# Performance work log

Hardware: AMD Instinct MI355X
Metric: run time of the kernel (lower is better)

## Reference

```python
import jax, jax.numpy as jnp
import numpy as np

B, C, H, W = 16, 192, 96, 96
FILTERS = (1, 3, 3, 3, 3, 1)  # (1,) + filters + (1,)
INIT_SCALE = 8.0
LIKELIHOOD_BOUND = 1e-9


def setup_inputs() -> dict:
    key = jax.random.key(0)
    ks = jax.random.split(key, 3)
    inp = {}
    inp["inputs"] = jax.random.normal(ks[0], (B, C, H, W), dtype=jnp.float32) * 4.0
    # uniform(-0.5, 0.5) quantization noise, supplied explicitly for determinism
    inp["noise"] = jax.random.uniform(ks[1], (B, C, H, W), dtype=jnp.float32) - 0.5
    scale = INIT_SCALE ** (1.0 / (len(FILTERS) - 1))  # 8 ** (1/5)
    for i in range(5):
        fin, fout = FILTERS[i], FILTERS[i + 1]
        init_m = float(np.log(np.expm1(1.0 / scale / fout)))
        inp[f"m{i}"] = jnp.full((C, fout, fin), init_m, dtype=jnp.float32)
        inp[f"b{i}"] = jax.random.uniform(
            jax.random.fold_in(ks[2], i), (C, fout, 1), dtype=jnp.float32,
            minval=-0.5, maxval=0.5)
        inp[f"f{i}"] = jnp.zeros((C, fout, 1), dtype=jnp.float32)
    return inp


@jax.custom_vjp
def low_bound(x):
    return jnp.clip(x, LIKELIHOOD_BOUND, None)

def _lb_fwd(x):
    return jnp.clip(x, LIKELIHOOD_BOUND, None), x

def _lb_bwd(x, g):
    # torch Low_bound: grad zeroed where x < 1e-9 (the t-mask is redundant after zeroing)
    return (jnp.where(x >= LIKELIHOOD_BOUND, g, jnp.zeros_like(g)),)

low_bound.defvjp(_lb_fwd, _lb_bwd)


def _logits_cumulative(x, mats, biases, factors):
    # x: (C, 1, N); each layer: batched tiny matmul + bias + tanh-factor gate
    for m, b, f in zip(mats, biases, factors):
        x = jnp.matmul(jax.nn.softplus(m), x) + b  # (C, f_out, N)
        x = x + jnp.tanh(f) * jnp.tanh(x)
    return x


def reference(inputs, noise, m0, m1, m2, m3, m4,
              b0, b1, b2, b3, b4, f0, f1, f2, f3, f4):
    mats = (m0, m1, m2, m3, m4)
    biases = (b0, b1, b2, b3, b4)
    factors = (f0, f1, f2, f3, f4)
    # permute (B,C,H,W) -> (C,B,H,W) -> (C, 1, B*H*W)
    x = jnp.transpose(inputs, (1, 0, 2, 3)).reshape(C, 1, -1)
    n = jnp.transpose(noise, (1, 0, 2, 3)).reshape(C, 1, -1)
    v = x + n  # 'noise' quantize mode
    lower = _logits_cumulative(v - 0.5, mats, biases, factors)
    upper = _logits_cumulative(v + 0.5, mats, biases, factors)
    sign = jax.lax.stop_gradient(-jnp.sign(lower + upper))
    likelihood = jnp.abs(jax.nn.sigmoid(sign * upper) - jax.nn.sigmoid(sign * lower))
    likelihood = low_bound(likelihood)
    outputs = jnp.transpose(v.reshape(C, B, H, W), (1, 0, 2, 3))
    likelihood = jnp.transpose(likelihood.reshape(C, B, H, W), (1, 0, 2, 3))
    return outputs, likelihood
```

## Files before the change

### kernel.cpp

```cpp
#include <hip/hip_runtime.h>
#include <math.h>

#define CC 192
#define BB 16
#define HWp 9216
#define NPLANES (BB * CC)
#define NELEM (BB * CC * HWp)

#define KLUT 2048
#define VMIN (-30.0f)
#define VMAX (30.0f)
#define DXLUT ((VMAX - VMIN) / (float)(KLUT - 1))
#define INV_DX ((float)(KLUT - 1) / (VMAX - VMIN))
#define OFFLUT (-VMIN * INV_DX)

__device__ __forceinline__ float fast_tanh(float x) {
    float e = __builtin_amdgcn_exp2f(x * 2.8853900817779268f);
    return 1.0f - 2.0f * __builtin_amdgcn_rcpf(e + 1.0f);
}

__device__ __forceinline__ float fast_sigmoid(float z) {
    float e = __builtin_amdgcn_exp2f(z * -1.4426950408889634f);
    return __builtin_amdgcn_rcpf(1.0f + e);
}

__device__ __forceinline__ float softplus_f(float x) {
    return (x > 20.0f) ? x : log1pf(expf(x));
}

struct Params {
    float W0[3], B0[3], T0[3];
    float W1[9], B1[3], T1[3];
    float W2[9], B2[3], T2[3];
    float W3[9], B3[3], T3[3];
    float W4[3], B4, T4;
};

#define EB_LAYER(OUT, IN, W, Bv, Tv)                                          \
    _Pragma("unroll")                                                         \
    for (int j = 0; j < 3; ++j) {                                             \
        float acc = fmaf((W)[j * 3 + 2], (IN)[2],                             \
                    fmaf((W)[j * 3 + 1], (IN)[1],                             \
                    fmaf((W)[j * 3 + 0], (IN)[0], (Bv)[j])));                 \
        (OUT)[j] = acc + (Tv)[j] * fast_tanh(acc);                            \
    }

__device__ __forceinline__ float chain(float u, const Params& P) {
    float h0[3], h1[3], h2[3], h3[3];
#pragma unroll
    for (int j = 0; j < 3; ++j) {
        float a = fmaf(P.W0[j], u, P.B0[j]);
        h0[j] = a + P.T0[j] * fast_tanh(a);
    }
    EB_LAYER(h1, h0, P.W1, P.B1, P.T1);
    EB_LAYER(h2, h1, P.W2, P.B2, P.T2);
    EB_LAYER(h3, h2, P.W3, P.B3, P.T3);
    float y = fmaf(P.W4[2], h3[2], fmaf(P.W4[1], h3[1], fmaf(P.W4[0], h3[0], P.B4)));
    y += P.T4 * fast_tanh(y);
    return y;
}

__device__ __forceinline__ float table_value(float v, const Params& P) {
    float lo = chain(v - 0.5f, P);
    float up = chain(v + 0.5f, P);
    float lk = fabsf(fast_sigmoid(up) - fast_sigmoid(lo));
    return fmaxf(lk, 1e-9f);
}

__device__ __forceinline__ void stage_params(
    int c, int t, float* sP,
    const float* m0, const float* b0, const float* f0,
    const float* m1, const float* b1, const float* f1,
    const float* m2, const float* b2, const float* f2,
    const float* m3, const float* b3, const float* f3,
    const float* m4, const float* b4, const float* f4)
{
    if (t < 59) {
        float val;
        if (t < 9) {
            int j = t % 3, w = t / 3;
            val = (w == 0) ? softplus_f(m0[c * 3 + j])
                : (w == 1) ? b0[c * 3 + j]
                           : tanhf(f0[c * 3 + j]);
        } else if (t < 54) {
            int u = t - 9;
            int l = u / 15, r = u % 15;
            const float* mm = (l == 0) ? m1 : (l == 1) ? m2 : m3;
            const float* bb = (l == 0) ? b1 : (l == 1) ? b2 : b3;
            const float* ff = (l == 0) ? f1 : (l == 1) ? f2 : f3;
            val = (r < 9)  ? softplus_f(mm[c * 9 + r])
                : (r < 12) ? bb[c * 3 + (r - 9)]
                           : tanhf(ff[c * 3 + (r - 12)]);
        } else {
            int r = t - 54;
            val = (r < 3)  ? softplus_f(m4[c * 3 + r])
                : (r == 3) ? b4[c]
                           : tanhf(f4[c]);
        }
        sP[t] = val;
    }
}

__device__ __forceinline__ void load_params(const float* sP, Params& P) {
#pragma unroll
    for (int j = 0; j < 3; ++j) { P.W0[j] = sP[j]; P.B0[j] = sP[3 + j]; P.T0[j] = sP[6 + j]; }
#pragma unroll
    for (int j = 0; j < 9; ++j) { P.W1[j] = sP[9 + j]; P.W2[j] = sP[24 + j]; P.W3[j] = sP[39 + j]; }
#pragma unroll
    for (int j = 0; j < 3; ++j) {
        P.B1[j] = sP[18 + j]; P.T1[j] = sP[21 + j];
        P.B2[j] = sP[33 + j]; P.T2[j] = sP[36 + j];
        P.B3[j] = sP[48 + j]; P.T3[j] = sP[51 + j];
        P.W4[j] = sP[54 + j];
    }
    P.B4 = sP[57];
    P.T4 = sP[58];
}

__device__ __forceinline__ float lut_lookup(const float* sT, float v) {
    float u = fmaf(v, INV_DX, OFFLUT);
    u = fminf(fmaxf(u, 0.0f), (float)(KLUT - 2) + 0.999f);
    float fi = floorf(u);
    float fr = u - fi;
    int i = (int)fi;
    float y0 = sT[i];
    float y1 = sT[i + 1];
    return fmaf(fr, y1 - y0, y0);
}

__global__ __launch_bounds__(256) void build_table(
    const float* __restrict__ m0, const float* __restrict__ b0, const float* __restrict__ f0,
    const float* __restrict__ m1, const float* __restrict__ b1, const float* __restrict__ f1,
    const float* __restrict__ m2, const float* __restrict__ b2, const float* __restrict__ f2,
    const float* __restrict__ m3, const float* __restrict__ b3, const float* __restrict__ f3,
    const float* __restrict__ m4, const float* __restrict__ b4, const float* __restrict__ f4,
    float* __restrict__ tab)
{
    const int c = blockIdx.x;
    const int t = threadIdx.x;
    __shared__ float sP[59];
    stage_params(c, t, sP, m0, b0, f0, m1, b1, f1, m2, b2, f2, m3, b3, f3, m4, b4, f4);
    __syncthreads();
    Params P;
    load_params(sP, P);
    for (int i = t; i < KLUT; i += 256) {
        float v = VMIN + (float)i * DXLUT;
        tab[(size_t)c * KLUT + i] = table_value(v, P);
    }
}

__global__ __launch_bounds__(256) void eb_main(
    const float* __restrict__ x, const float* __restrict__ nz,
    const float* __restrict__ tab, float* __restrict__ out)
{
    const int plane = blockIdx.x;
    const int c = plane % CC;
    const int t = threadIdx.x;

    __shared__ float sT[KLUT];
    {
        const float4* tv = (const float4*)(tab + (size_t)c * KLUT);
        float4* sv = (float4*)sT;
#pragma unroll
        for (int i = 0; i < KLUT / 4 / 256; ++i)
            sv[t + i * 256] = tv[t + i * 256];
    }
    __syncthreads();

    const size_t base = (size_t)plane * HWp;
    const float4* xv = (const float4*)(x + base);
    const float4* nv = (const float4*)(nz + base);
    float4* ov = (float4*)(out + base);
    float4* lv = (float4*)(out + (size_t)NELEM + base);

    for (int i = t; i < HWp / 4; i += 256) {
        float4 a = xv[i];
        float4 n = nv[i];
        float4 v, lk;
        v.x = a.x + n.x;  v.y = a.y + n.y;  v.z = a.z + n.z;  v.w = a.w + n.w;
        lk.x = lut_lookup(sT, v.x);
        lk.y = lut_lookup(sT, v.y);
        lk.z = lut_lookup(sT, v.z);
        lk.w = lut_lookup(sT, v.w);
        ov[i] = v;
        lv[i] = lk;
    }
}

__global__ __launch_bounds__(256) void eb_fused(
    const float* __restrict__ x, const float* __restrict__ nz,
    const float* __restrict__ m0, const float* __restrict__ b0, const float* __restrict__ f0,
    const float* __restrict__ m1, const float* __restrict__ b1, const float* __restrict__ f1,
    const float* __restrict__ m2, const float* __restrict__ b2, const float* __restrict__ f2,
    const float* __restrict__ m3, const float* __restrict__ b3, const float* __restrict__ f3,
    const float* __restrict__ m4, const float* __restrict__ b4, const float* __restrict__ f4,
    float* __restrict__ out)
{
    const int plane = blockIdx.x;
    const int c = plane % CC;
    const int t = threadIdx.x;

    __shared__ float sP[59];
    __shared__ float sT[KLUT];
    stage_params(c, t, sP, m0, b0, f0, m1, b1, f1, m2, b2, f2, m3, b3, f3, m4, b4, f4);
    __syncthreads();
    {
        Params P;
        load_params(sP, P);
#pragma unroll
        for (int k = 0; k < KLUT / 256; ++k) {
            int i = t + k * 256;
            float v = VMIN + (float)i * DXLUT;
            sT[i] = table_value(v, P);
        }
    }
    __syncthreads();

    const size_t base = (size_t)plane * HWp;
    const float4* xv = (const float4*)(x + base);
    const float4* nv = (const float4*)(nz + base);
    float4* ov = (float4*)(out + base);
    float4* lv = (float4*)(out + (size_t)NELEM + base);

    for (int i = t; i < HWp / 4; i += 256) {
        float4 a = xv[i];
        float4 n = nv[i];
        float4 v, lk;
        v.x = a.x + n.x;  v.y = a.y + n.y;  v.z = a.z + n.z;  v.w = a.w + n.w;
        lk.x = lut_lookup(sT, v.x);
        lk.y = lut_lookup(sT, v.y);
        lk.z = lut_lookup(sT, v.z);
        lk.w = lut_lookup(sT, v.w);
        ov[i] = v;
        lv[i] = lk;
    }
}

extern "C" void kernel_launch(void* const* d_in, const int* in_sizes, int n_in,
                              void* d_out, int out_size, void* d_ws, size_t ws_size,
                              hipStream_t stream) {
    const float* x  = (const float*)d_in[0];
    const float* nz = (const float*)d_in[1];
    const float* m0 = (const float*)d_in[2];
    const float* b0 = (const float*)d_in[3];
    const float* f0 = (const float*)d_in[4];
    const float* m1 = (const float*)d_in[5];
    const float* b1 = (const float*)d_in[6];
    const float* f1 = (const float*)d_in[7];
    const float* m2 = (const float*)d_in[8];
    const float* b2 = (const float*)d_in[9];
    const float* f2 = (const float*)d_in[10];
    const float* m3 = (const float*)d_in[11];
    const float* b3 = (const float*)d_in[12];
    const float* f3 = (const float*)d_in[13];
    const float* m4 = (const float*)d_in[14];
    const float* b4 = (const float*)d_in[15];
    const float* f4 = (const float*)d_in[16];
    float* out = (float*)d_out;

    const size_t tab_bytes = (size_t)CC * KLUT * sizeof(float);
    if (ws_size >= tab_bytes) {
        float* tab = (float*)d_ws;
        build_table<<<CC, 256, 0, stream>>>(
            m0, b0, f0, m1, b1, f1, m2, b2, f2, m3, b3, f3, m4, b4, f4, tab);
        eb_main<<<NPLANES, 256, 0, stream>>>(x, nz, tab, out);
    } else {
        eb_fused<<<NPLANES, 256, 0, stream>>>(x, nz,
            m0, b0, f0, m1, b1, f1, m2, b2, f2, m3, b3, f3, m4, b4, f4, out);
    }
}
```

Baseline: 419.1 us.

## Pair LUT entries, halve table size, process two planes per block with nontemporal IO

Shrinks the lookup table to 1024 entries and stores each entry as an adjacent (y0,y1) float2 pair, so every interpolation needs one LDS read instead of two. The main kernel now uses a 2D grid in which each block handles two batch planes of the same channel, so the table is staged into LDS half as many times. Loads and stores become nontemporal vector accesses with a fixed-trip, partially unrolled loop. The coarser table lowers interpolation accuracy, and there are fewer, larger blocks in the grid.

New measurement: 400.7 us. -4.4%, faster.

```diff
diff --git a/kernel.cpp b/kernel.cpp
--- a/kernel.cpp
+++ b/kernel.cpp
@@ -7,12 +7,14 @@
 #define NPLANES (BB * CC)
 #define NELEM (BB * CC * HWp)
 
-#define KLUT 2048
+#define KLUT 1024
 #define VMIN (-30.0f)
 #define VMAX (30.0f)
 #define DXLUT ((VMAX - VMIN) / (float)(KLUT - 1))
 #define INV_DX ((float)(KLUT - 1) / (VMAX - VMIN))
 #define OFFLUT (-VMIN * INV_DX)
+
+typedef float fvec4 __attribute__((ext_vector_type(4)));
 
 __device__ __forceinline__ float fast_tanh(float x) {
     float e = __builtin_amdgcn_exp2f(x * 2.8853900817779268f);
@@ -117,15 +119,13 @@
     P.T4 = sP[58];
 }
 
-__device__ __forceinline__ float lut_lookup(const float* sT, float v) {
+__device__ __forceinline__ float lut_lookup(const float2* sT, float v) {
     float u = fmaf(v, INV_DX, OFFLUT);
-    u = fminf(fmaxf(u, 0.0f), (float)(KLUT - 2) + 0.999f);
+    u = fminf(fmaxf(u, 0.0f), (float)(KLUT - 1));
     float fi = floorf(u);
     float fr = u - fi;
-    int i = (int)fi;
-    float y0 = sT[i];
-    float y1 = sT[i + 1];
-    return fmaf(fr, y1 - y0, y0);
+    float2 y = sT[(int)fi];
+    return fmaf(fr, y.y - y.x, y.x);
 }
 
 __global__ __launch_bounds__(256) void build_table(
@@ -134,56 +134,79 @@
     const float* __restrict__ m2, const float* __restrict__ b2, const float* __restrict__ f2,
     const float* __restrict__ m3, const float* __restrict__ b3, const float* __restrict__ f3,
     const float* __restrict__ m4, const float* __restrict__ b4, const float* __restrict__ f4,
-    float* __restrict__ tab)
+    float2* __restrict__ tab2)
 {
     const int c = blockIdx.x;
     const int t = threadIdx.x;
     __shared__ float sP[59];
+    __shared__ float sY[KLUT];
     stage_params(c, t, sP, m0, b0, f0, m1, b1, f1, m2, b2, f2, m3, b3, f3, m4, b4, f4);
     __syncthreads();
     Params P;
     load_params(sP, P);
-    for (int i = t; i < KLUT; i += 256) {
-        float v = VMIN + (float)i * DXLUT;
-        tab[(size_t)c * KLUT + i] = table_value(v, P);
+#pragma unroll
+    for (int k = 0; k < KLUT / 256; ++k) {
+        int i = t + k * 256;
+        sY[i] = table_value(VMIN + (float)i * DXLUT, P);
+    }
+    __syncthreads();
+#pragma unroll
+    for (int k = 0; k < KLUT / 256; ++k) {
+        int i = t + k * 256;
+        float y0 = sY[i];
+        float y1 = sY[(i + 1 < KLUT) ? i + 1 : KLUT - 1];
+        tab2[(size_t)c * KLUT + i] = make_float2(y0, y1);
     }
 }
 
 __global__ __launch_bounds__(256) void eb_main(
     const float* __restrict__ x, const float* __restrict__ nz,
-    const float* __restrict__ tab, float* __restrict__ out)
-{
-    const int plane = blockIdx.x;
-    const int c = plane % CC;
+    const float2* __restrict__ tab2, float* __restrict__ out)
+{
+    const int c = blockIdx.x;
+    const int q = blockIdx.y;
     const int t = threadIdx.x;
 
-    __shared__ float sT[KLUT];
+    __shared__ float2 sT[KLUT];
     {
-        const float4* tv = (const float4*)(tab + (size_t)c * KLUT);
-        float4* sv = (float4*)sT;
-#pragma unroll
-        for (int i = 0; i < KLUT / 4 / 256; ++i)
-            sv[t + i * 256] = tv[t + i * 256];
-    }
-    __syncthreads();
-
-    const size_t base = (size_t)plane * HWp;
-    const float4* xv = (const float4*)(x + base);
-    const float4* nv = (const float4*)(nz + base);
-    float4* ov = (float4*)(out + base);
-    float4* lv = (float4*)(out + (size_t)NELEM + base);
-
-    for (int i = t; i < HWp / 4; i += 256) {
-        float4 a = xv[i];
-        float4 n = nv[i];
-        float4 v, lk;
-        v.x = a.x + n.x;  v.y = a.y + n.y;  v.z = a.z + n.z;  v.w = a.w + n.w;
-        lk.x = lut_lookup(sT, v.x);
-        lk.y = lut_lookup(sT, v.y);
-        lk.z = lut_lookup(sT, v.z);
-        lk.w = lut_lookup(sT, v.w);
-        ov[i] = v;
-        lv[i] = lk;
+        const fvec4* tv = (const fvec4*)(tab2 + (size_t)c * KLUT);
+        fvec4* sv = (fvec4*)sT;
+#pragma unroll
+        for (int k = 0; k < (KLUT * 2 / 4) / 256; ++k)
+            sv[t + k * 256] = tv[t + k * 256];
+    }
+    __syncthreads();
+
+    const size_t base0 = ((size_t)(2 * q) * CC + c) * HWp;
+    const size_t base1 = base0 + (size_t)CC * HWp;
+
+    const fvec4* xv0 = (const fvec4*)(x + base0);
+    const fvec4* nv0 = (const fvec4*)(nz + base0);
+    fvec4* ov0 = (fvec4*)(out + base0);
+    fvec4* lv0 = (fvec4*)(out + (size_t)NELEM + base0);
+    const fvec4* xv1 = (const fvec4*)(x + base1);
+    const fvec4* nv1 = (const fvec4*)(nz + base1);
+    fvec4* ov1 = (fvec4*)(out + base1);
+    fvec4* lv1 = (fvec4*)(out + (size_t)NELEM + base1);
+
+#pragma unroll 3
+    for (int k = 0; k < (HWp / 4) / 256; ++k) {
+        int i = t + k * 256;
+        fvec4 a0 = __builtin_nontemporal_load(xv0 + i);
+        fvec4 n0 = __builtin_nontemporal_load(nv0 + i);
+        fvec4 a1 = __builtin_nontemporal_load(xv1 + i);
+        fvec4 n1 = __builtin_nontemporal_load(nv1 + i);
+        fvec4 v0 = a0 + n0;
+        fvec4 v1 = a1 + n1;
+        fvec4 l0, l1;
+        l0.x = lut_lookup(sT, v0.x);  l0.y = lut_lookup(sT, v0.y);
+        l0.z = lut_lookup(sT, v0.z);  l0.w = lut_lookup(sT, v0.w);
+        l1.x = lut_lookup(sT, v1.x);  l1.y = lut_lookup(sT, v1.y);
+        l1.z = lut_lookup(sT, v1.z);  l1.w = lut_lookup(sT, v1.w);
+        __builtin_nontemporal_store(v0, ov0 + i);
+        __builtin_nontemporal_store(l0, lv0 + i);
+        __builtin_nontemporal_store(v1, ov1 + i);
+        __builtin_nontemporal_store(l1, lv1 + i);
     }
 }
 
@@ -201,7 +224,8 @@
     const int t = threadIdx.x;
 
     __shared__ float sP[59];
-    __shared__ float sT[KLUT];
+    __shared__ float sY[KLUT];
+    __shared__ float2 sT[KLUT];
     stage_params(c, t, sP, m0, b0, f0, m1, b1, f1, m2, b2, f2, m3, b3, f3, m4, b4, f4);
     __syncthreads();
     {
@@ -210,29 +234,33 @@
 #pragma unroll
         for (int k = 0; k < KLUT / 256; ++k) {
             int i = t + k * 256;
-            float v = VMIN + (float)i * DXLUT;
-            sT[i] = table_value(v, P);
+            sY[i] = table_value(VMIN + (float)i * DXLUT, P);
         }
     }
     __syncthreads();
+#pragma unroll
+    for (int k = 0; k < KLUT / 256; ++k) {
+        int i = t + k * 256;
+        sT[i] = make_float2(sY[i], sY[(i + 1 < KLUT) ? i + 1 : KLUT - 1]);
+    }
+    __syncthreads();
 
     const size_t base = (size_t)plane * HWp;
-    const float4* xv = (const float4*)(x + base);
-    const float4* nv = (const float4*)(nz + base);
-    float4* ov = (float4*)(out + base);
-    float4* lv = (float4*)(out + (size_t)NELEM + base);
-
-    for (int i = t; i < HWp / 4; i += 256) {
-        float4 a = xv[i];
-        float4 n = nv[i];
-        float4 v, lk;
-        v.x = a.x + n.x;  v.y = a.y + n.y;  v.z = a.z + n.z;  v.w = a.w + n.w;
-        lk.x = lut_lookup(sT, v.x);
-        lk.y = lut_lookup(sT, v.y);
-        lk.z = lut_lookup(sT, v.z);
-        lk.w = lut_lookup(sT, v.w);
-        ov[i] = v;
-        lv[i] = lk;
+    const fvec4* xv = (const fvec4*)(x + base);
+    const fvec4* nv = (const fvec4*)(nz + base);
+    fvec4* ov = (fvec4*)(out + base);
+    fvec4* lv = (fvec4*)(out + (size_t)NELEM + base);
+
+    for (int k = 0; k < (HWp / 4) / 256; ++k) {
+        int i = t + k * 256;
+        fvec4 a = __builtin_nontemporal_load(xv + i);
+        fvec4 n = __builtin_nontemporal_load(nv + i);
+        fvec4 v = a + n;
+        fvec4 lk;
+        lk.x = lut_lookup(sT, v.x);  lk.y = lut_lookup(sT, v.y);
+        lk.z = lut_lookup(sT, v.z);  lk.w = lut_lookup(sT, v.w);
+        __builtin_nontemporal_store(v, ov + i);
+        __builtin_nontemporal_store(lk, lv + i);
     }
 }
 
@@ -258,12 +286,12 @@
     const float* f4 = (const float*)d_in[16];
     float* out = (float*)d_out;
 
-    const size_t tab_bytes = (size_t)CC * KLUT * sizeof(float);
+    const size_t tab_bytes = (size_t)CC * KLUT * sizeof(float2);
     if (ws_size >= tab_bytes) {
-        float* tab = (float*)d_ws;
+        float2* tab2 = (float2*)d_ws;
         build_table<<<CC, 256, 0, stream>>>(
-            m0, b0, f0, m1, b1, f1, m2, b2, f2, m3, b3, f3, m4, b4, f4, tab);
-        eb_main<<<NPLANES, 256, 0, stream>>>(x, nz, tab, out);
+            m0, b0, f0, m1, b1, f1, m2, b2, f2, m3, b3, f3, m4, b4, f4, tab2);
+        eb_main<<<dim3(CC, BB / 2), 256, 0, stream>>>(x, nz, tab2, out);
     } else {
         eb_fused<<<NPLANES, 256, 0, stream>>>(x, nz,
             m0, b0, f0, m1, b1, f1, m2, b2, f2, m3, b3, f3, m4, b4, f4, out);
```
